# Optimization experiments

Measured on AMD Instinct MI355X. Metric: run time of the kernel, lower is better.

The kernel has to match this reference:

```python
import jax, jax.numpy as jnp
import numpy as np

S, DIM, H, HD = 8192, 1280, 16, 80
B, L = 8, 1024  # 8 equal-length packed segments


def setup_inputs() -> dict:
    key = jax.random.key(0)
    ks = jax.random.split(key, 6)
    hidden_states = jax.random.normal(ks[0], (S, DIM), dtype=jnp.float32)
    Wqkv = jax.random.normal(ks[1], (DIM, 3 * DIM), dtype=jnp.float32) * (DIM ** -0.5)
    bqkv = jax.random.normal(ks[2], (3 * DIM,), dtype=jnp.float32) * 0.02
    Wproj = jax.random.normal(ks[3], (DIM, DIM), dtype=jnp.float32) * (DIM ** -0.5)
    bproj = jax.random.normal(ks[4], (DIM,), dtype=jnp.float32) * 0.02
    # rotary tables: per-token position within its segment, repeated-half layout
    pos = jnp.tile(jnp.arange(L, dtype=jnp.float32), B)  # [S]
    inv_freq = 1.0 / (10000.0 ** (jnp.arange(0, HD, 2, dtype=jnp.float32) / HD))  # [HD/2]
    ang = pos[:, None] * inv_freq[None, :]  # [S, HD/2]
    ang = jnp.concatenate([ang, ang], axis=-1)  # [S, HD]
    cos, sin = jnp.cos(ang), jnp.sin(ang)
    cu_seqlens = (jnp.arange(B + 1, dtype=jnp.int32) * L)
    return {"hidden_states": hidden_states, "cos": cos, "sin": sin,
            "Wqkv": Wqkv, "bqkv": bqkv, "Wproj": Wproj, "bproj": bproj,
            "cu_seqlens": cu_seqlens, "max_seqlen": L}


def _rotate_half(x):
    x1, x2 = jnp.split(x, 2, axis=-1)
    return jnp.concatenate([-x2, x1], axis=-1)


def reference(hidden_states, cos, sin, Wqkv, bqkv, Wproj, bproj, cu_seqlens, max_seqlen):
    s = hidden_states.shape[0]
    nseg = cu_seqlens.shape[0] - 1
    scale = HD ** -0.5
    qkv = (hidden_states @ Wqkv + bqkv).reshape(s, 3, H, HD)
    q, k, v = qkv[:, 0], qkv[:, 1], qkv[:, 2]  # each [S, H, HD]
    c = cos[:, None, :]
    sn = sin[:, None, :]
    q = q * c + _rotate_half(q) * sn
    k = k * c + _rotate_half(k) * sn
    # equal-length packed segments: [S,H,HD] -> [B,L,H,HD]
    q = q.reshape(nseg, max_seqlen, H, HD)
    k = k.reshape(nseg, max_seqlen, H, HD)
    v = v.reshape(nseg, max_seqlen, H, HD)
    scores = jnp.einsum("blhd,bmhd->bhlm", q, k) * scale
    probs = jax.nn.softmax(scores, axis=-1)
    out = jnp.einsum("bhlm,bmhd->blhd", probs, v).reshape(s, DIM)
    return out @ Wproj + bproj
```

## Files before the change

kernel.cpp:

```cpp
#include <hip/hip_runtime.h>
#include <hip/hip_bf16.h>
#include <stdint.h>

typedef __bf16 bf16_t;
typedef __bf16 bf16x8 __attribute__((ext_vector_type(8)));
typedef float f32x4 __attribute__((ext_vector_type(4)));
typedef float f32x16 __attribute__((ext_vector_type(16)));

#define S_TOK 8192
#define DIM   1280
#define NH    16
#define HD    80
#define LSEQ  1024
#define N_QKV 3840

__device__ __forceinline__ void gload16(const bf16_t* g, void* l) {
  __builtin_amdgcn_global_load_lds(
      (__attribute__((address_space(1))) uint32_t*)g,
      (__attribute__((address_space(3))) uint32_t*)l, 16, 0, 0);
}

__global__ __launch_bounds__(256) void k_conv_bf16(const float* __restrict__ in,
                                                   bf16_t* __restrict__ out) {
  int g = blockIdx.x * 256 + threadIdx.x;
  const float4* p = reinterpret_cast<const float4*>(in) + (size_t)g * 2;
  float4 v0 = p[0], v1 = p[1];
  bf16x8 o;
  o[0] = (bf16_t)v0.x; o[1] = (bf16_t)v0.y; o[2] = (bf16_t)v0.z; o[3] = (bf16_t)v0.w;
  o[4] = (bf16_t)v1.x; o[5] = (bf16_t)v1.y; o[6] = (bf16_t)v1.z; o[7] = (bf16_t)v1.w;
  *reinterpret_cast<bf16x8*>(out + (size_t)g * 8) = o;
}

__global__ __launch_bounds__(256) void k_transpose_bf16(const float* __restrict__ W,
                                                        bf16_t* __restrict__ Wt,
                                                        int K, int N) {
  __shared__ float tile[32][33];
  int n0 = blockIdx.x * 32, k0 = blockIdx.y * 32;
  int tx = threadIdx.x, ty = threadIdx.y;
#pragma unroll
  for (int j = 0; j < 32; j += 8)
    tile[ty + j][tx] = W[(size_t)(k0 + ty + j) * N + n0 + tx];
  __syncthreads();
#pragma unroll
  for (int j = 0; j < 32; j += 8)
    Wt[(size_t)(n0 + ty + j) * K + k0 + tx] = (bf16_t)tile[tx][ty + j];
}

template <bool OUT_BF16>
__global__ __launch_bounds__(512, 2) void k_gemm8(const bf16_t* __restrict__ A,
                                                  const bf16_t* __restrict__ Bt,
                                                  const float* __restrict__ bias,
                                                  void* __restrict__ Cout,
                                                  int N) {
  constexpr int K = 1280;
  constexpr int NT = K / 64;
  __shared__ __align__(16) char smem[131072];
  const int nb = N >> 8;
  const int cpx = (int)gridDim.x >> 3;
  const int wg = ((int)blockIdx.x & 7) * cpx + ((int)blockIdx.x >> 3);
  const int bm = wg / nb, bn = wg % nb;
  const int tid = threadIdx.x, lane = tid & 63, w = tid >> 6;
  const int wm = w >> 2, wn = w & 3;
  const int l15 = lane & 15, lg = lane >> 4;

  const bf16_t* Ab = A + (size_t)(bm * 256) * K;
  const bf16_t* Bb = Bt + (size_t)(bn * 256) * K;

  const int srow = w * 8 + (lane >> 3);
  const int scol = ((lane & 7) ^ (lane >> 3)) * 8;

  float bv4[4];
#pragma unroll
  for (int nf = 0; nf < 4; ++nf)
    bv4[nf] = bias[bn * 256 + wn * 64 + nf * 16 + l15];
  asm volatile("" :: "v"(bv4[0]), "v"(bv4[1]), "v"(bv4[2]), "v"(bv4[3]) : "memory");

  char* const sm = smem;
  auto stageA = [&](int buf, int g, int k0) {
    gload16(Ab + (size_t)(g * 64 + srow) * K + k0 + scol,
            sm + buf * 65536 + g * 8192 + w * 1024);
  };
  auto stageB = [&](int buf, int g, int k0) {
    gload16(Bb + (size_t)(g * 64 + srow) * K + k0 + scol,
            sm + buf * 65536 + 32768 + g * 8192 + w * 1024);
  };

  f32x4 acc[8][4];
#pragma unroll
  for (int i = 0; i < 8; ++i)
#pragma unroll
    for (int j = 0; j < 4; ++j) acc[i][j] = (f32x4){0.f, 0.f, 0.f, 0.f};

#pragma unroll
  for (int g = 0; g < 4; ++g) { stageA(0, g, 0); stageB(0, g, 0); }
  asm volatile("s_waitcnt vmcnt(0)\n\ts_barrier" ::: "memory");

#pragma unroll 1
  for (int T = 0; T < NT; ++T) {
    const int buf = T & 1, nbuf = buf ^ 1;
    const int k1 = (T + 1) * 64;
    if (T + 1 < NT) {
#pragma unroll
      for (int g = 0; g < 4; ++g) { stageA(nbuf, g, k1); stageB(nbuf, g, k1); }
    }
    const char* Abase = sm + buf * 65536;
    const char* Bbase = Abase + 32768;
#pragma unroll
    for (int kk = 0; kk < 2; ++kk) {
      const int cb = kk * 64 + lg * 16;
      bf16x8 bfv[4];
#pragma unroll
      for (int nf = 0; nf < 4; ++nf) {
        const int row = wn * 64 + nf * 16 + l15;
        bfv[nf] = *reinterpret_cast<const bf16x8*>(Bbase + row * 128 + (cb ^ ((row & 7) << 4)));
      }
#pragma unroll
      for (int mg = 0; mg < 2; ++mg) {
        bf16x8 af[4];
#pragma unroll
        for (int mf = 0; mf < 4; ++mf) {
          const int row = wm * 128 + mg * 64 + mf * 16 + l15;
          af[mf] = *reinterpret_cast<const bf16x8*>(Abase + row * 128 + (cb ^ ((row & 7) << 4)));
        }
        __builtin_amdgcn_s_setprio(1);
#pragma unroll
        for (int mf = 0; mf < 4; ++mf)
#pragma unroll
          for (int nf = 0; nf < 4; ++nf)
            acc[mg * 4 + mf][nf] =
                __builtin_amdgcn_mfma_f32_16x16x32_bf16(af[mf], bfv[nf], acc[mg * 4 + mf][nf], 0, 0, 0);
        __builtin_amdgcn_s_setprio(0);
      }
    }
    if (T + 1 < NT) {
      asm volatile("s_waitcnt vmcnt(0)\n\ts_barrier" ::: "memory");
    }
  }

  const int rg = lg << 2;
#pragma unroll
  for (int nf = 0; nf < 4; ++nf) {
    const int col = bn * 256 + wn * 64 + nf * 16 + l15;
    const float bv = bv4[nf];
#pragma unroll
    for (int m8 = 0; m8 < 8; ++m8) {
      const int row0 = bm * 256 + wm * 128 + m8 * 16 + rg;
#pragma unroll
      for (int r = 0; r < 4; ++r) {
        float v = acc[m8][nf][r] + bv;
        if (OUT_BF16)
          reinterpret_cast<bf16_t*>(Cout)[(size_t)(row0 + r) * N + col] = (bf16_t)v;
        else
          reinterpret_cast<float*>(Cout)[(size_t)(row0 + r) * N + col] = v;
      }
    }
  }
}

__global__ __launch_bounds__(256) void k_rope(bf16_t* __restrict__ qkv,
                                              const float* __restrict__ cosT,
                                              const float* __restrict__ sinT) {
  const float QS = 0.11180339887498949f * 1.4426950408889634f;
  int g = blockIdx.x * 256 + threadIdx.x;
  int c = g % 5;
  int h = (g / 5) & 15;
  int s = g / 80;
  const int d0 = c * 8;
  float cs[8], sn[8];
#pragma unroll
  for (int j = 0; j < 8; ++j) {
    cs[j] = cosT[s * 80 + d0 + j];
    sn[j] = sinT[s * 80 + d0 + j];
  }
  size_t base = (size_t)s * N_QKV + h * 80 + d0;
#pragma unroll
  for (int part = 0; part < 2; ++part) {
    const float sc = (part == 0) ? QS : 1.0f;
    bf16_t* p0 = qkv + base + part * 1280;
    bf16_t* p1 = p0 + 40;
    bf16x8 a = *reinterpret_cast<bf16x8*>(p0);
    bf16x8 b = *reinterpret_cast<bf16x8*>(p1);
    bf16x8 oa, ob;
#pragma unroll
    for (int j = 0; j < 8; ++j) {
      float x = (float)a[j], y = (float)b[j];
      oa[j] = (bf16_t)((x * cs[j] - y * sn[j]) * sc);
      ob[j] = (bf16_t)((y * cs[j] + x * sn[j]) * sc);
    }
    *reinterpret_cast<bf16x8*>(p0) = oa;
    *reinterpret_cast<bf16x8*>(p1) = ob;
  }
}

__global__ __launch_bounds__(256) void k_vtrans(const bf16_t* __restrict__ qkv,
                                                bf16_t* __restrict__ vtg) {
  __shared__ bf16_t T[64][88];
  int sh = blockIdx.x >> 4;
  int kt = blockIdx.x & 15;
  int seg = sh >> 4, h = sh & 15;
  int kv0 = kt * 64;
  int tid = threadIdx.x;
#pragma unroll
  for (int i = 0; i < 3; ++i) {
    int c = tid + i * 256;
    if (c < 640) {
      int r = c / 10, ch = c - r * 10;
      *reinterpret_cast<uint4*>(&T[r][ch * 8]) =
        *reinterpret_cast<const uint4*>(qkv + (size_t)(seg * 1024 + kv0 + r) * N_QKV + 2 * DIM + h * 80 + ch * 8);
    }
  }
  __syncthreads();
#pragma unroll
  for (int i = 0; i < 3; ++i) {
    int c = tid + i * 256;
    if (c < 640) {
      int d = c >> 3, co = c & 7;
      bf16x8 o;
#pragma unroll
      for (int j = 0; j < 8; ++j) {
        int kp = co * 8 + j;
        int kv = (kp & ~12) | (((kp >> 2) & 1) << 3) | (((kp >> 3) & 1) << 2);
        o[j] = T[kv][d];
      }
      *reinterpret_cast<bf16x8*>(vtg + ((size_t)(sh * 80 + d)) * 1024 + kv0 + co * 8) = o;
    }
  }
}

__global__ __launch_bounds__(512, 2) void k_attn2(const bf16_t* __restrict__ qkv,
                                                  const bf16_t* __restrict__ vtg,
                                                  bf16_t* __restrict__ outp) {
  __shared__ __align__(16) char smem[69632];
  bf16_t* KsB = (bf16_t*)smem;
  bf16_t* VsB = (bf16_t*)(smem + 32768);

  const int bid = blockIdx.x;
  const int seg = bid & 7, qt = (bid >> 3) & 3, h = bid >> 5;
  const int tid = threadIdx.x, lane = tid & 63, w = tid >> 6;
  const int l31 = lane & 31, hi = lane >> 5;
  const int sw = l31 & 7;
  const int q0 = seg * 1024 + qt * 256;

  const bf16_t* kbase = qkv + ((size_t)seg * 1024) * N_QKV + DIM + h * 80;
  const bf16_t* vbase = vtg + ((size_t)(seg * 16 + h) * 80) * 1024;

  bf16x8 qf[5];
  {
    const bf16_t* qp = qkv + (size_t)(q0 + w * 32 + l31) * N_QKV + h * 80 + hi * 8;
#pragma unroll
    for (int ks = 0; ks < 5; ++ks) qf[ks] = *reinterpret_cast<const bf16x8*>(qp + ks * 16);
  }

  const uint4 ones4 = {0x3F803F80u, 0x3F803F80u, 0x3F803F80u, 0x3F803F80u};
  uint4 kreg[2], vreg[2];
  auto issue = [&](int kv0) {
#pragma unroll
    for (int i = 0; i < 2; ++i) {
      int c = tid + i * 512;
      if (c < 640) {
        int r = c / 10, ch = c - r * 10;
        kreg[i] = *reinterpret_cast<const uint4*>(kbase + (size_t)(kv0 + r) * N_QKV + ch * 8);
      }
    }
#pragma unroll
    for (int i = 0; i < 2; ++i) {
      int c = tid + i * 512;
      if (c < 768) {
        int d = c >> 3, ch = c & 7;
        uint4 v = {0u, 0u, 0u, 0u};
        if (d < 80) v = *reinterpret_cast<const uint4*>(vbase + (size_t)d * 1024 + kv0 + ch * 8);
        else if (d == 80) v = ones4;
        vreg[i] = v;
      }
    }
  };
  auto commit = [&](int kb, int vb) {
    bf16_t* Kb = KsB + kb * 8192;
    bf16_t* Vb = VsB + vb * 6144;
#pragma unroll
    for (int i = 0; i < 2; ++i) {
      int c = tid + i * 512;
      if (c < 640) {
        int r = c / 10, ch = c - r * 10;
        *reinterpret_cast<uint4*>(Kb + r * 128 + ((ch ^ (r & 7)) << 3)) = kreg[i];
      }
    }
#pragma unroll
    for (int i = 0; i < 2; ++i) {
      int c = tid + i * 512;
      if (c < 768) {
        int d = c >> 3, ch = c & 7;
        *reinterpret_cast<uint4*>(Vb + d * 64 + ((ch ^ (d & 7)) << 3)) = vreg[i];
      }
    }
  };

  f32x16 o0, o1, o2;
#pragma unroll
  for (int r = 0; r < 16; ++r) { o0[r] = 0.f; o1[r] = 0.f; o2[r] = 0.f; }
  float mrun = -1e30f;
  f32x16 st0, st1;
  bf16x8 pb[4];

  auto qk = [&](int kb) {
#pragma unroll
    for (int r = 0; r < 16; ++r) { st0[r] = 0.f; st1[r] = 0.f; }
    const bf16_t* Kb = KsB + kb * 8192;
    __builtin_amdgcn_s_setprio(1);
#pragma unroll
    for (int ks = 0; ks < 5; ++ks) {
      const int so = (((ks << 1) | hi) ^ sw) << 3;
      bf16x8 k0 = *reinterpret_cast<const bf16x8*>(Kb + l31 * 128 + so);
      bf16x8 k1 = *reinterpret_cast<const bf16x8*>(Kb + (32 + l31) * 128 + so);
      st0 = __builtin_amdgcn_mfma_f32_32x32x16_bf16(k0, qf[ks], st0, 0, 0, 0);
      st1 = __builtin_amdgcn_mfma_f32_32x32x16_bf16(k1, qf[ks], st1, 0, 0, 0);
    }
    __builtin_amdgcn_s_setprio(0);
  };
  auto pv = [&](int vb) {
    const bf16_t* Vb = VsB + vb * 6144;
    __builtin_amdgcn_s_setprio(1);
#pragma unroll
    for (int ks2 = 0; ks2 < 4; ++ks2) {
      const int so = (((ks2 << 1) | hi) ^ sw) << 3;
      bf16x8 v0 = *reinterpret_cast<const bf16x8*>(Vb + l31 * 64 + so);
      bf16x8 v1 = *reinterpret_cast<const bf16x8*>(Vb + (32 + l31) * 64 + so);
      bf16x8 v2 = *reinterpret_cast<const bf16x8*>(Vb + (64 + l31) * 64 + so);
      o0 = __builtin_amdgcn_mfma_f32_32x32x16_bf16(v0, pb[ks2], o0, 0, 0, 0);
      o1 = __builtin_amdgcn_mfma_f32_32x32x16_bf16(v1, pb[ks2], o1, 0, 0, 0);
      o2 = __builtin_amdgcn_mfma_f32_32x32x16_bf16(v2, pb[ks2], o2, 0, 0, 0);
    }
    __builtin_amdgcn_s_setprio(0);
  };
  auto softmax_pack = [&]() {
    float mt[16];
#pragma unroll
    for (int r = 0; r < 16; ++r) mt[r] = fmaxf(st0[r], st1[r]);
#pragma unroll
    for (int s2 = 8; s2 >= 1; s2 >>= 1)
#pragma unroll
      for (int r = 0; r < s2; ++r) mt[r] = fmaxf(mt[r], mt[r + s2]);
    float mx = fmaxf(mt[0], __shfl_xor(mt[0], 32));
    if (!__all(mx <= mrun + 6.0f)) {
      float mnew = fmaxf(mrun, mx);
      float corr = __builtin_exp2f(mrun - mnew);
      mrun = mnew;
#pragma unroll
      for (int r = 0; r < 16; ++r) { o0[r] *= corr; o1[r] *= corr; o2[r] *= corr; }
    }
#pragma unroll
    for (int r = 0; r < 16; ++r) st0[r] = __builtin_exp2f(st0[r] - mrun);
#pragma unroll
    for (int r = 0; r < 16; ++r) st1[r] = __builtin_exp2f(st1[r] - mrun);
#pragma unroll
    for (int u = 0; u < 2; ++u)
#pragma unroll
      for (int j = 0; j < 8; ++j) {
        pb[u][j]     = (bf16_t)st0[u * 8 + j];
        pb[2 + u][j] = (bf16_t)st1[u * 8 + j];
      }
  };

  issue(0);
  commit(0, 0);
  __syncthreads();
  issue(64);
  qk(0);
  softmax_pack();
  commit(1, 1);
  __syncthreads();

#pragma unroll 1
  for (int t = 1; t < 16; ++t) {
    if (t < 15) issue((t + 1) * 64);
    qk(t & 1);
    pv((t - 1) % 3);
    softmax_pack();
    if (t < 15) commit((t + 1) & 1, (t + 1) % 3);
    __syncthreads();
  }
  pv(0);
  __syncthreads();

  float sp = o2[8] + __shfl_xor(o2[8], 32);
  float inv = 1.0f / sp;

  bf16_t* Osm = (bf16_t*)smem;
  const int qrow = w * 32 + l31;
#pragma unroll
  for (int r = 0; r < 16; ++r) {
    int crow = (r & 3) + 8 * (r >> 2) + 4 * hi;
    Osm[qrow * 88 + crow]      = (bf16_t)(o0[r] * inv);
    Osm[qrow * 88 + 32 + crow] = (bf16_t)(o1[r] * inv);
    if (r < 8) Osm[qrow * 88 + 64 + crow] = (bf16_t)(o2[r] * inv);
  }
  __syncthreads();
#pragma unroll
  for (int i = 0; i < 5; ++i) {
    int c = tid + i * 512;
    int q = c / 10, ch = c - q * 10;
    uint4 v = *reinterpret_cast<const uint4*>(Osm + q * 88 + ch * 8);
    *reinterpret_cast<uint4*>(outp + (size_t)(q0 + q) * DIM + h * 80 + ch * 8) = v;
  }
}

extern "C" void kernel_launch(void* const* d_in, const int* in_sizes, int n_in,
                              void* d_out, int out_size, void* d_ws, size_t ws_size,
                              hipStream_t stream) {
  const float* hs    = (const float*)d_in[0];
  const float* cosT  = (const float*)d_in[1];
  const float* sinT  = (const float*)d_in[2];
  const float* Wqkv  = (const float*)d_in[3];
  const float* bqkv  = (const float*)d_in[4];
  const float* Wproj = (const float*)d_in[5];
  const float* bproj = (const float*)d_in[6];
  (void)in_sizes; (void)n_in; (void)out_size; (void)ws_size;

  char* ws = (char*)d_ws;
  bf16_t* hsb  = (bf16_t*)(ws);
  bf16_t* w1t  = (bf16_t*)(ws + 20971520);
  bf16_t* w2t  = (bf16_t*)(ws + 30801920);
  bf16_t* qkvb = (bf16_t*)(ws + 34078720);
  bf16_t* attn = (bf16_t*)(ws + 96993280);
  bf16_t* vtg  = hsb;

  k_conv_bf16<<<5120, 256, 0, stream>>>(hs, hsb);
  k_transpose_bf16<<<dim3(120, 40), dim3(32, 8), 0, stream>>>(Wqkv, w1t, 1280, 3840);
  k_transpose_bf16<<<dim3(40, 40), dim3(32, 8), 0, stream>>>(Wproj, w2t, 1280, 1280);
  k_gemm8<true><<<480, 512, 0, stream>>>(hsb, w1t, bqkv, (void*)qkvb, 3840);
  k_rope<<<2560, 256, 0, stream>>>(qkvb, cosT, sinT);
  k_vtrans<<<2048, 256, 0, stream>>>(qkvb, vtg);
  k_attn2<<<512, 512, 0, stream>>>(qkvb, vtg, attn);
  k_gemm8<false><<<160, 512, 0, stream>>>(attn, w2t, bproj, d_out, 1280);
}
```

Measured before the change: 254.5 us.

## Fuse RoPE into QKV GEMM epilogue via interleaved q/k column permutation

Removes the standalone RoPE kernel by permuting the weight rows loaded for q/k so that each rotary pair lands in adjacent output columns. The rotation and q scaling are then applied in the GEMM epilogue with a lane xor-shuffle. This eliminates a full read-modify-write pass over the q/k activations and one launch. In exchange, the epilogue does extra per-element cos/sin loads, and the stored q/k head dims are interleaved rather than in the original order, which stays consistent only because q and k share the permutation.

```diff
diff --git a/kernel.cpp b/kernel.cpp
--- a/kernel.cpp
+++ b/kernel.cpp
@@ -13,6 +13,12 @@
 #define HD    80
 #define LSEQ  1024
 #define N_QKV 3840
+
+__device__ __forceinline__ int qk_perm(int n) {
+  if (n >= 2560) return n;
+  int base = (n / 80) * 80, j = n - base;
+  return base + ((j & 1) ? (j >> 1) + 40 : (j >> 1));
+}
 
 __device__ __forceinline__ void gload16(const bf16_t* g, void* l) {
   __builtin_amdgcn_global_load_lds(
@@ -46,14 +52,17 @@
     Wt[(size_t)(n0 + ty + j) * K + k0 + tx] = (bf16_t)tile[tx][ty + j];
 }
 
-template <bool OUT_BF16>
+template <bool OUT_BF16, bool ROPE>
 __global__ __launch_bounds__(512, 2) void k_gemm8(const bf16_t* __restrict__ A,
                                                   const bf16_t* __restrict__ Bt,
                                                   const float* __restrict__ bias,
                                                   void* __restrict__ Cout,
-                                                  int N) {
+                                                  int N,
+                                                  const float* __restrict__ cosT,
+                                                  const float* __restrict__ sinT) {
   constexpr int K = 1280;
   constexpr int NT = K / 64;
+  const float QS = 0.11180339887498949f * 1.4426950408889634f;
   __shared__ __align__(16) char smem[131072];
   const int nb = N >> 8;
   const int cpx = (int)gridDim.x >> 3;
@@ -64,15 +73,23 @@
   const int l15 = lane & 15, lg = lane >> 4;
 
   const bf16_t* Ab = A + (size_t)(bm * 256) * K;
-  const bf16_t* Bb = Bt + (size_t)(bn * 256) * K;
 
   const int srow = w * 8 + (lane >> 3);
   const int scol = ((lane & 7) ^ (lane >> 3)) * 8;
 
+  int srowB[4];
+#pragma unroll
+  for (int g = 0; g < 4; ++g) {
+    int n = bn * 256 + g * 64 + srow;
+    srowB[g] = ROPE ? qk_perm(n) : n;
+  }
+
   float bv4[4];
 #pragma unroll
-  for (int nf = 0; nf < 4; ++nf)
-    bv4[nf] = bias[bn * 256 + wn * 64 + nf * 16 + l15];
+  for (int nf = 0; nf < 4; ++nf) {
+    int col = bn * 256 + wn * 64 + nf * 16 + l15;
+    bv4[nf] = bias[ROPE ? qk_perm(col) : col];
+  }
   asm volatile("" :: "v"(bv4[0]), "v"(bv4[1]), "v"(bv4[2]), "v"(bv4[3]) : "memory");
 
   char* const sm = smem;
@@ -81,7 +98,7 @@
             sm + buf * 65536 + g * 8192 + w * 1024);
   };
   auto stageB = [&](int buf, int g, int k0) {
-    gload16(Bb + (size_t)(g * 64 + srow) * K + k0 + scol,
+    gload16(Bt + (size_t)srowB[g] * K + k0 + scol,
             sm + buf * 65536 + 32768 + g * 8192 + w * 1024);
   };
 
@@ -142,53 +159,31 @@
   for (int nf = 0; nf < 4; ++nf) {
     const int col = bn * 256 + wn * 64 + nf * 16 + l15;
     const float bv = bv4[nf];
+    const bool isqk = ROPE && (col < 2560);
+    const bool isq  = col < 1280;
+    const int pi = (col % 80) >> 1;
+    const float sgn = (l15 & 1) ? 1.f : -1.f;
 #pragma unroll
     for (int m8 = 0; m8 < 8; ++m8) {
       const int row0 = bm * 256 + wm * 128 + m8 * 16 + rg;
 #pragma unroll
       for (int r = 0; r < 4; ++r) {
         float v = acc[m8][nf][r] + bv;
+        if (isqk) {
+          const int row = row0 + r;
+          float other = __shfl_xor(v, 1);
+          float c = cosT[(size_t)row * 80 + pi];
+          float s = sinT[(size_t)row * 80 + pi];
+          v = v * c + sgn * other * s;
+          if (isq) v *= QS;
+        }
+        const int orow = row0 + r;
         if (OUT_BF16)
-          reinterpret_cast<bf16_t*>(Cout)[(size_t)(row0 + r) * N + col] = (bf16_t)v;
+          reinterpret_cast<bf16_t*>(Cout)[(size_t)orow * N + col] = (bf16_t)v;
         else
-          reinterpret_cast<float*>(Cout)[(size_t)(row0 + r) * N + col] = v;
-      }
-    }
-  }
-}
-
-__global__ __launch_bounds__(256) void k_rope(bf16_t* __restrict__ qkv,
-                                              const float* __restrict__ cosT,
-                                              const float* __restrict__ sinT) {
-  const float QS = 0.11180339887498949f * 1.4426950408889634f;
-  int g = blockIdx.x * 256 + threadIdx.x;
-  int c = g % 5;
-  int h = (g / 5) & 15;
-  int s = g / 80;
-  const int d0 = c * 8;
-  float cs[8], sn[8];
-#pragma unroll
-  for (int j = 0; j < 8; ++j) {
-    cs[j] = cosT[s * 80 + d0 + j];
-    sn[j] = sinT[s * 80 + d0 + j];
-  }
-  size_t base = (size_t)s * N_QKV + h * 80 + d0;
-#pragma unroll
-  for (int part = 0; part < 2; ++part) {
-    const float sc = (part == 0) ? QS : 1.0f;
-    bf16_t* p0 = qkv + base + part * 1280;
-    bf16_t* p1 = p0 + 40;
-    bf16x8 a = *reinterpret_cast<bf16x8*>(p0);
-    bf16x8 b = *reinterpret_cast<bf16x8*>(p1);
-    bf16x8 oa, ob;
-#pragma unroll
-    for (int j = 0; j < 8; ++j) {
-      float x = (float)a[j], y = (float)b[j];
-      oa[j] = (bf16_t)((x * cs[j] - y * sn[j]) * sc);
-      ob[j] = (bf16_t)((y * cs[j] + x * sn[j]) * sc);
-    }
-    *reinterpret_cast<bf16x8*>(p0) = oa;
-    *reinterpret_cast<bf16x8*>(p1) = ob;
+          reinterpret_cast<float*>(Cout)[(size_t)orow * N + col] = v;
+      }
+    }
   }
 }
 
@@ -427,9 +422,8 @@
   k_conv_bf16<<<5120, 256, 0, stream>>>(hs, hsb);
   k_transpose_bf16<<<dim3(120, 40), dim3(32, 8), 0, stream>>>(Wqkv, w1t, 1280, 3840);
   k_transpose_bf16<<<dim3(40, 40), dim3(32, 8), 0, stream>>>(Wproj, w2t, 1280, 1280);
-  k_gemm8<true><<<480, 512, 0, stream>>>(hsb, w1t, bqkv, (void*)qkvb, 3840);
-  k_rope<<<2560, 256, 0, stream>>>(qkvb, cosT, sinT);
+  k_gemm8<true, true><<<480, 512, 0, stream>>>(hsb, w1t, bqkv, (void*)qkvb, 3840, cosT, sinT);
   k_vtrans<<<2048, 256, 0, stream>>>(qkvb, vtg);
   k_attn2<<<512, 512, 0, stream>>>(qkvb, vtg, attn);
-  k_gemm8<false><<<160, 512, 0, stream>>>(attn, w2t, bproj, d_out, 1280);
-}
+  k_gemm8<false, false><<<160, 512, 0, stream>>>(attn, w2t, bproj, d_out, 1280, nullptr, nullptr);
+}
```

After: 299.4 us. +17.6%, slower.
